# Performance work log

Measured on AMD Instinct MI355X. Metric: run time of the kernel, lower is better.

Reference implementation:

```python
import jax, jax.numpy as jnp
import numpy as np

EMBED_DIM = 1024
ATTN_DIM = 1024


def setup_inputs() -> dict:
    key = jax.random.key(0)
    k1, k2, k3, k4 = jax.random.split(key, 4)
    embedded = jax.random.normal(k1, (4, 2048, EMBED_DIM), dtype=jnp.float32)
    # torch nn.Linear weights are [out_features, in_features]
    s = 1.0 / np.sqrt(EMBED_DIM)
    Wk = jax.random.uniform(k2, (ATTN_DIM, EMBED_DIM), jnp.float32, -s, s)
    Wq = jax.random.uniform(k3, (ATTN_DIM, EMBED_DIM), jnp.float32, -s, s)
    Wv = jax.random.uniform(k4, (ATTN_DIM, EMBED_DIM), jnp.float32, -s, s)
    return {"embedded": embedded, "Wk": Wk, "Wq": Wq, "Wv": Wv}


def reference(embedded, Wk, Wq, Wv):
    # projections: x @ W.T  (torch Linear, no bias)
    k = jnp.einsum("bse,ae->bsa", embedded, Wk)
    q = jnp.einsum("bse,ae->bsa", embedded, Wq)
    v = jnp.einsum("bse,ae->bsa", embedded, Wv)
    scale = 1.0 / jnp.sqrt(jnp.float32(ATTN_DIM))
    attn = jnp.einsum("bqa,bka->bqk", q, k) * scale  # [B, S, S]
    S = attn.shape[1]
    causal = jnp.tril(jnp.ones((S, S), dtype=bool))
    attn = jnp.where(causal[None, :, :], attn, -jnp.inf)
    a = jax.nn.softmax(attn, axis=2)
    out = jnp.einsum("bqk,bka->bqa", a, v)
    return jnp.round(out, 4)
```

## Files before the change

kernel.cpp:

```cpp
#include <hip/hip_runtime.h>
#include <hip/hip_bf16.h>
#include <hip/hip_fp16.h>
#include <stdint.h>

typedef __bf16 bf16_t;
typedef bf16_t bf16x8 __attribute__((ext_vector_type(8)));
typedef bf16_t bf16x4 __attribute__((ext_vector_type(4)));
typedef _Float16 f16x8 __attribute__((ext_vector_type(8)));
typedef float f32x4 __attribute__((ext_vector_type(4)));

#define BM 128
#define BN 128
#define BK 32

__device__ __forceinline__ void gload_lds16(const void* g, void* l) {
    __builtin_amdgcn_global_load_lds(
        (const __attribute__((address_space(1))) void*)(uintptr_t)g,
        (__attribute__((address_space(3))) void*)(uintptr_t)l,
        16, 0, 0);
}

template <int EPI>
__device__ __forceinline__ void gemm_body(
    const bf16_t* __restrict__ A, long lda,
    const bf16_t* __restrict__ B, long ldb,
    void* __restrict__ Cv, long ldc,
    int k0beg, int k1end, float scale, int m0, int n0)
{
    __shared__ __align__(16) bf16_t As[BM * BK];
    __shared__ __align__(16) bf16_t Bs[BN * BK];

    const int tid = threadIdx.x;
    const int wid = tid >> 6, lane = tid & 63;
    const int wr = wid >> 1, wc = wid & 1;
    const int hw = lane >> 4, ln = lane & 15;

    const int ar0 = tid >> 2,         ak0 = (tid & 3) * 8;
    const int ar1 = (tid + 256) >> 2, ak1 = (tid & 3) * 8;

    const bf16_t* Arow0 = A + (size_t)(m0 + ar0) * lda + ak0;
    const bf16_t* Arow1 = A + (size_t)(m0 + ar1) * lda + ak1;
    const bf16_t* Brow0 = B + (size_t)(n0 + ar0) * ldb + ak0;
    const bf16_t* Brow1 = B + (size_t)(n0 + ar1) * ldb + ak1;

    f32x4 acc[4][4] = {};

    for (int k0 = k0beg; k0 < k1end; k0 += BK) {
        gload_lds16(Arow0 + k0, &As[wid * 512]);
        gload_lds16(Arow1 + k0, &As[2048 + wid * 512]);
        gload_lds16(Brow0 + k0, &Bs[wid * 512]);
        gload_lds16(Brow1 + k0, &Bs[2048 + wid * 512]);
        __syncthreads();

        bf16x8 af[4], bfr[4];
#pragma unroll
        for (int t = 0; t < 4; t++) {
            af[t]  = *(const bf16x8*)&As[(wr * 64 + t * 16 + ln) * BK + hw * 8];
            bfr[t] = *(const bf16x8*)&Bs[(wc * 64 + t * 16 + ln) * BK + hw * 8];
        }
#pragma unroll
        for (int ti = 0; ti < 4; ti++)
#pragma unroll
            for (int tj = 0; tj < 4; tj++)
                acc[ti][tj] = __builtin_amdgcn_mfma_f32_16x16x32_bf16(
                    af[ti], bfr[tj], acc[ti][tj], 0, 0, 0);
        __syncthreads();
    }

#pragma unroll
    for (int ti = 0; ti < 4; ti++) {
        const int rbase = m0 + wr * 64 + ti * 16 + hw * 4;
#pragma unroll
        for (int tj = 0; tj < 4; tj++) {
            const int col = n0 + wc * 64 + tj * 16 + ln;
#pragma unroll
            for (int rg = 0; rg < 4; rg++) {
                const float v = acc[ti][tj][rg] * scale;
                const size_t idx = (size_t)(rbase + rg) * ldc + col;
                if (EPI == 0)      ((bf16_t*)Cv)[idx]   = (bf16_t)v;
                else if (EPI == 1) ((_Float16*)Cv)[idx] = (_Float16)v;
                else               ((float*)Cv)[idx]    = v;
            }
        }
    }
}

__global__ __launch_bounds__(256) void gemm1_qkv(
    const bf16_t* __restrict__ xb, const bf16_t* __restrict__ Wb,
    bf16_t* __restrict__ QKVb)
{
    const int lin = blockIdx.x;
    const int xcd = lin & 7;
    const int j   = lin >> 3;
    const int p   = j >> 6;
    const int w   = j & 63;
    const int mblk = xcd * 8 + (w >> 3);
    const int nblk = p * 8 + (w & 7);
    gemm_body<0>(xb, 1024, Wb, 1024, QKVb, 3072,
                 0, 1024, 1.0f, mblk * BM, nblk * BN);
}

__global__ __launch_bounds__(256) void qk_vtrans(
    const bf16_t* __restrict__ QKVb, _Float16* __restrict__ S,
    bf16_t* __restrict__ Vt)
{
    const int id = blockIdx.x;
    if (id < 1024) {
        const int b  = id & 3;
        const int g  = id >> 2;
        const int my = 15 - (g >> 4);
        const int nx = g & 15;
        const int m0 = my * BM, n0 = nx * BN;
        if (n0 > m0 + (BM - 1)) return;
        const bf16_t* Qb = QKVb + 1024 + (size_t)b * (2048L * 3072);
        const bf16_t* Kb = QKVb + (size_t)b * (2048L * 3072);
        _Float16* Sb = S + (size_t)b * (2048L * 2048);
        gemm_body<1>(Qb, 3072, Kb, 3072, Sb, 2048, 0, 1024, 0.03125f, m0, n0);
    } else {
        __shared__ bf16_t ttile[32][33];
        const int t = id - 1024;
        const int b = t >> 11;
        const int lin = t & 2047;
        const int s0 = (lin & 63) * 32;
        const int d0 = (lin >> 6) * 32;
        const int tx = threadIdx.x & 31, ty = threadIdx.x >> 5;
#pragma unroll
        for (int k = 0; k < 4; k++) {
            const int s = s0 + ty + k * 8;
            const int d = d0 + tx;
            ttile[ty + k * 8][tx] = QKVb[(size_t)(b * 2048 + s) * 3072 + 2048 + d];
        }
        __syncthreads();
#pragma unroll
        for (int k = 0; k < 4; k++) {
            const int d = d0 + ty + k * 8;
            const int s = s0 + tx;
            Vt[(size_t)b * (1024 * 2048) + (size_t)d * 2048 + s] = ttile[tx][ty + k * 8];
        }
    }
}

__global__ __launch_bounds__(256) void gemm3_pv(
    const bf16_t* __restrict__ P, const bf16_t* __restrict__ Vt,
    float* __restrict__ out)
{
    const int id = blockIdx.x;
    const int strip = 15 - (id >> 5);
    const int nx = (id >> 2) & 7;
    const int b = id & 3;
    const int m0 = strip * BM;
    const int Keff = m0 + BM;
    gemm_body<2>(P + (size_t)b * (2048L * 2048), 2048,
                 Vt + (size_t)b * (1024L * 2048), 2048,
                 out + (size_t)b * (2048L * 1024), 1024,
                 0, Keff, 1.0f, m0, nx * BN);
}

__global__ __launch_bounds__(256) void cast_all(
    const float* __restrict__ x,
    const float* __restrict__ Wk, const float* __restrict__ Wq,
    const float* __restrict__ Wv,
    bf16_t* __restrict__ xb, bf16_t* __restrict__ Wb)
{
    const int blk = blockIdx.x;
    const float* src;
    bf16_t* dst;
    if (blk < 8192) {
        const size_t i = ((size_t)blk * 256 + threadIdx.x) * 4;
        src = x + i;
        dst = xb + i;
    } else {
        const size_t j = ((size_t)(blk - 8192) * 256 + threadIdx.x) * 4;
        dst = Wb + j;
        if (j < (size_t)1048576)      src = Wk + j;
        else if (j < (size_t)2097152) src = Wq + (j - 1048576);
        else                          src = Wv + (j - 2097152);
    }
    const float4 v = *(const float4*)src;
    bf16x4 o;
    o.x = (bf16_t)v.x; o.y = (bf16_t)v.y; o.z = (bf16_t)v.z; o.w = (bf16_t)v.w;
    *(bf16x4*)dst = o;
}

__device__ __forceinline__ float wred_max(float v) {
#pragma unroll
    for (int o = 32; o; o >>= 1) v = fmaxf(v, __shfl_xor(v, o, 64));
    return v;
}
__device__ __forceinline__ float wred_sum(float v) {
#pragma unroll
    for (int o = 32; o; o >>= 1) v += __shfl_xor(v, o, 64);
    return v;
}

__global__ __launch_bounds__(256) void softmax_rows(_Float16* __restrict__ S)
{
    __shared__ float red[8];
    const int r = blockIdx.x;
    const int i = r & 2047;
    const int n = i + 1;
    _Float16* row = S + (size_t)r * 2048;
    const int tid = threadIdx.x;
    const int wid = tid >> 6, lane = tid & 63;
    const int base = tid * 8;

    const f16x8 v8 = *(const f16x8*)(row + base);
    float vals[8];
    float mx = -3e30f;
#pragma unroll
    for (int k = 0; k < 8; k++) {
        const float v = (base + k < n) ? (float)v8[k] : -3e30f;
        vals[k] = v;
        mx = fmaxf(mx, v);
    }
    mx = wred_max(mx);
    if (lane == 0) red[wid] = mx;
    __syncthreads();
    mx = fmaxf(fmaxf(red[0], red[1]), fmaxf(red[2], red[3]));

    float s = 0.f;
#pragma unroll
    for (int k = 0; k < 8; k++) {
        const float e = __expf(vals[k] - mx);
        vals[k] = e;
        s += e;
    }
    s = wred_sum(s);
    if (lane == 0) red[4 + wid] = s;
    __syncthreads();
    s = red[4] + red[5] + red[6] + red[7];
    const float inv = 1.0f / s;

    bf16x8 o;
#pragma unroll
    for (int k = 0; k < 8; k++) o[k] = (bf16_t)(vals[k] * inv);
    *(bf16x8*)((bf16_t*)row + base) = o;
}

extern "C" void kernel_launch(void* const* d_in, const int* in_sizes, int n_in,
                              void* d_out, int out_size, void* d_ws, size_t ws_size,
                              hipStream_t stream)
{
    const float* x  = (const float*)d_in[0];
    const float* Wk = (const float*)d_in[1];
    const float* Wq = (const float*)d_in[2];
    const float* Wv = (const float*)d_in[3];
    char* ws = (char*)d_ws;

    bf16_t*   QKVb = (bf16_t*)(ws);
    bf16_t*   Vt   = (bf16_t*)(ws + ((size_t)48 << 20));
    bf16_t*   xb   = (bf16_t*)(ws + ((size_t)64 << 20));
    bf16_t*   Wb   = (bf16_t*)(ws + ((size_t)80 << 20));
    _Float16* S    = (_Float16*)(ws + ((size_t)64 << 20));
    float*    out  = (float*)d_out;

    cast_all<<<11264, 256, 0, stream>>>(x, Wk, Wq, Wv, xb, Wb);

    gemm1_qkv<<<1536, 256, 0, stream>>>(xb, Wb, QKVb);

    qk_vtrans<<<9216, 256, 0, stream>>>(QKVb, S, Vt);

    softmax_rows<<<8192, 256, 0, stream>>>(S);

    gemm3_pv<<<512, 256, 0, stream>>>((bf16_t*)S, Vt, out);
}
```

Measured before the change: 243.5 us.

## Widen GEMM tiles to 128x256, swizzle LDS, fuse V transpose into QKV epilogue

Widens the shared GEMM tile from 128x128 to 128x256, so each wave now computes 4x8 MFMA tiles, and adds an XOR-style rotation to the LDS layout to reduce bank conflicts. The V projection is written transposed straight from the QKV GEMM epilogue, which removes the separate transpose pass and the write and reread of V. The QK kernel now launches only causally needed tiles instead of launching all tiles and exiting early. The trade-offs are more accumulator registers, hence launch_bounds(256,2), and fewer blocks per launch, which may leave parts of the GPU idle.

```diff
diff --git a/kernel.cpp b/kernel.cpp
--- a/kernel.cpp
+++ b/kernel.cpp
@@ -10,7 +10,7 @@
 typedef float f32x4 __attribute__((ext_vector_type(4)));
 
 #define BM 128
-#define BN 128
+#define BN 256
 #define BK 32
 
 __device__ __forceinline__ void gload_lds16(const void* g, void* l) {
@@ -35,33 +35,48 @@
     const int wr = wid >> 1, wc = wid & 1;
     const int hw = lane >> 4, ln = lane & 15;
 
-    const int ar0 = tid >> 2,         ak0 = (tid & 3) * 8;
-    const int ar1 = (tid + 256) >> 2, ak1 = (tid & 3) * 8;
-
-    const bf16_t* Arow0 = A + (size_t)(m0 + ar0) * lda + ak0;
-    const bf16_t* Arow1 = A + (size_t)(m0 + ar1) * lda + ak1;
-    const bf16_t* Brow0 = B + (size_t)(n0 + ar0) * ldb + ak0;
-    const bf16_t* Brow1 = B + (size_t)(n0 + ar1) * ldb + ak1;
-
-    f32x4 acc[4][4] = {};
+    const bf16_t* srcA[2];
+#pragma unroll
+    for (int i = 0; i < 2; i++) {
+        const int c = tid + i * 256;
+        const int row = c >> 2;
+        const int j = ((c & 3) - (row >> 1)) & 3;
+        srcA[i] = A + (size_t)(m0 + row) * lda + j * 8;
+    }
+    const bf16_t* srcB[4];
+#pragma unroll
+    for (int q = 0; q < 4; q++) {
+        const int c = tid + q * 256;
+        const int row = c >> 2;
+        const int j = ((c & 3) - (row >> 1)) & 3;
+        srcB[q] = B + (size_t)(n0 + row) * ldb + j * 8;
+    }
+
+    f32x4 acc[4][8] = {};
 
     for (int k0 = k0beg; k0 < k1end; k0 += BK) {
-        gload_lds16(Arow0 + k0, &As[wid * 512]);
-        gload_lds16(Arow1 + k0, &As[2048 + wid * 512]);
-        gload_lds16(Brow0 + k0, &Bs[wid * 512]);
-        gload_lds16(Brow1 + k0, &Bs[2048 + wid * 512]);
+        gload_lds16(srcA[0] + k0, &As[wid * 512]);
+        gload_lds16(srcA[1] + k0, &As[2048 + wid * 512]);
+#pragma unroll
+        for (int q = 0; q < 4; q++)
+            gload_lds16(srcB[q] + k0, &Bs[q * 2048 + wid * 512]);
         __syncthreads();
 
-        bf16x8 af[4], bfr[4];
+        bf16x8 af[4], bfr[8];
 #pragma unroll
         for (int t = 0; t < 4; t++) {
-            af[t]  = *(const bf16x8*)&As[(wr * 64 + t * 16 + ln) * BK + hw * 8];
-            bfr[t] = *(const bf16x8*)&Bs[(wc * 64 + t * 16 + ln) * BK + hw * 8];
+            const int r = wr * 64 + t * 16 + ln;
+            af[t] = *(const bf16x8*)&As[r * BK + (((hw + (r >> 1)) & 3) * 8)];
         }
 #pragma unroll
+        for (int u = 0; u < 8; u++) {
+            const int rb = wc * 128 + u * 16 + ln;
+            bfr[u] = *(const bf16x8*)&Bs[rb * BK + (((hw + (rb >> 1)) & 3) * 8)];
+        }
+#pragma unroll
         for (int ti = 0; ti < 4; ti++)
 #pragma unroll
-            for (int tj = 0; tj < 4; tj++)
+            for (int tj = 0; tj < 8; tj++)
                 acc[ti][tj] = __builtin_amdgcn_mfma_f32_16x16x32_bf16(
                     af[ti], bfr[tj], acc[ti][tj], 0, 0, 0);
         __syncthreads();
@@ -71,89 +86,80 @@
     for (int ti = 0; ti < 4; ti++) {
         const int rbase = m0 + wr * 64 + ti * 16 + hw * 4;
 #pragma unroll
-        for (int tj = 0; tj < 4; tj++) {
-            const int col = n0 + wc * 64 + tj * 16 + ln;
-#pragma unroll
-            for (int rg = 0; rg < 4; rg++) {
-                const float v = acc[ti][tj][rg] * scale;
-                const size_t idx = (size_t)(rbase + rg) * ldc + col;
-                if (EPI == 0)      ((bf16_t*)Cv)[idx]   = (bf16_t)v;
-                else if (EPI == 1) ((_Float16*)Cv)[idx] = (_Float16)v;
-                else               ((float*)Cv)[idx]    = v;
+        for (int tj = 0; tj < 8; tj++) {
+            const int col = n0 + wc * 128 + tj * 16 + ln;
+            if (EPI == 4) {
+                const int bb = rbase >> 11;
+                const int s  = rbase & 2047;
+                const int d  = col - 2048;
+                bf16x4 o;
+#pragma unroll
+                for (int rg = 0; rg < 4; rg++) o[rg] = (bf16_t)acc[ti][tj][rg];
+                *(bf16x4*)&((bf16_t*)Cv)[(size_t)bb * 2097152 + (size_t)d * 2048 + s] = o;
+            } else {
+#pragma unroll
+                for (int rg = 0; rg < 4; rg++) {
+                    const float v = acc[ti][tj][rg] * scale;
+                    const size_t idx = (size_t)(rbase + rg) * ldc + col;
+                    if (EPI == 0)      ((bf16_t*)Cv)[idx]   = (bf16_t)v;
+                    else if (EPI == 1) ((_Float16*)Cv)[idx] = (_Float16)v;
+                    else               ((float*)Cv)[idx]    = v;
+                }
             }
         }
     }
 }
 
-__global__ __launch_bounds__(256) void gemm1_qkv(
+__global__ __launch_bounds__(256, 2) void gemm1_qkv(
     const bf16_t* __restrict__ xb, const bf16_t* __restrict__ Wb,
-    bf16_t* __restrict__ QKVb)
+    bf16_t* __restrict__ QKVb, bf16_t* __restrict__ Vt)
 {
     const int lin = blockIdx.x;
     const int xcd = lin & 7;
     const int j   = lin >> 3;
-    const int p   = j >> 6;
-    const int w   = j & 63;
-    const int mblk = xcd * 8 + (w >> 3);
-    const int nblk = p * 8 + (w & 7);
-    gemm_body<0>(xb, 1024, Wb, 1024, QKVb, 3072,
-                 0, 1024, 1.0f, mblk * BM, nblk * BN);
-}
-
-__global__ __launch_bounds__(256) void qk_vtrans(
-    const bf16_t* __restrict__ QKVb, _Float16* __restrict__ S,
-    bf16_t* __restrict__ Vt)
-{
-    const int id = blockIdx.x;
-    if (id < 1024) {
-        const int b  = id & 3;
-        const int g  = id >> 2;
-        const int my = 15 - (g >> 4);
-        const int nx = g & 15;
-        const int m0 = my * BM, n0 = nx * BN;
-        if (n0 > m0 + (BM - 1)) return;
-        const bf16_t* Qb = QKVb + 1024 + (size_t)b * (2048L * 3072);
-        const bf16_t* Kb = QKVb + (size_t)b * (2048L * 3072);
-        _Float16* Sb = S + (size_t)b * (2048L * 2048);
-        gemm_body<1>(Qb, 3072, Kb, 3072, Sb, 2048, 0, 1024, 0.03125f, m0, n0);
-    } else {
-        __shared__ bf16_t ttile[32][33];
-        const int t = id - 1024;
-        const int b = t >> 11;
-        const int lin = t & 2047;
-        const int s0 = (lin & 63) * 32;
-        const int d0 = (lin >> 6) * 32;
-        const int tx = threadIdx.x & 31, ty = threadIdx.x >> 5;
-#pragma unroll
-        for (int k = 0; k < 4; k++) {
-            const int s = s0 + ty + k * 8;
-            const int d = d0 + tx;
-            ttile[ty + k * 8][tx] = QKVb[(size_t)(b * 2048 + s) * 3072 + 2048 + d];
-        }
-        __syncthreads();
-#pragma unroll
-        for (int k = 0; k < 4; k++) {
-            const int d = d0 + ty + k * 8;
-            const int s = s0 + tx;
-            Vt[(size_t)b * (1024 * 2048) + (size_t)d * 2048 + s] = ttile[tx][ty + k * 8];
-        }
-    }
-}
-
-__global__ __launch_bounds__(256) void gemm3_pv(
+    const int p   = j >> 5;
+    const int w   = j & 31;
+    const int mblk = xcd * 8 + (w >> 2);
+    const int nblk = p * 4 + (w & 3);
+    const int m0 = mblk * BM, n0 = nblk * BN;
+    if (nblk < 8)
+        gemm_body<0>(xb, 1024, Wb, 1024, QKVb, 2048, 0, 1024, 1.0f, m0, n0);
+    else
+        gemm_body<4>(xb, 1024, Wb, 1024, Vt, 2048, 0, 1024, 1.0f, m0, n0);
+}
+
+__global__ __launch_bounds__(256, 2) void qk_gemm(
+    const bf16_t* __restrict__ QKVb, _Float16* __restrict__ S)
+{
+    const int b = blockIdx.x & 3;
+    int rem = blockIdx.x >> 2;
+    int my = 15, nx2 = 0;
+#pragma unroll
+    for (int m = 15; m >= 0; --m) {
+        const int c = (m >> 1) + 1;
+        if (rem < c) { my = m; nx2 = rem; break; }
+        rem -= c;
+    }
+    const bf16_t* base = QKVb + (size_t)b * (2048L * 2048);
+    gemm_body<1>(base + 1024, 2048,
+                 base, 2048,
+                 S + (size_t)b * (2048L * 2048), 2048,
+                 0, 1024, 0.03125f, my * BM, nx2 * BN);
+}
+
+__global__ __launch_bounds__(256, 2) void gemm3_pv(
     const bf16_t* __restrict__ P, const bf16_t* __restrict__ Vt,
     float* __restrict__ out)
 {
-    const int id = blockIdx.x;
-    const int strip = 15 - (id >> 5);
-    const int nx = (id >> 2) & 7;
-    const int b = id & 3;
+    const int b = blockIdx.x & 3;
+    const int g = blockIdx.x >> 2;
+    const int strip = 15 - (g >> 2);
+    const int nx2 = g & 3;
     const int m0 = strip * BM;
-    const int Keff = m0 + BM;
     gemm_body<2>(P + (size_t)b * (2048L * 2048), 2048,
                  Vt + (size_t)b * (1024L * 2048), 2048,
                  out + (size_t)b * (2048L * 1024), 1024,
-                 0, Keff, 1.0f, m0, nx * BN);
+                 0, m0 + BM, 1.0f, m0, nx2 * BN);
 }
 
 __global__ __launch_bounds__(256) void cast_all(
@@ -248,19 +254,19 @@
     char* ws = (char*)d_ws;
 
     bf16_t*   QKVb = (bf16_t*)(ws);
-    bf16_t*   Vt   = (bf16_t*)(ws + ((size_t)48 << 20));
-    bf16_t*   xb   = (bf16_t*)(ws + ((size_t)64 << 20));
-    bf16_t*   Wb   = (bf16_t*)(ws + ((size_t)80 << 20));
-    _Float16* S    = (_Float16*)(ws + ((size_t)64 << 20));
+    bf16_t*   Vt   = (bf16_t*)(ws + ((size_t)32 << 20));
+    bf16_t*   xb   = (bf16_t*)(ws + ((size_t)48 << 20));
+    bf16_t*   Wb   = (bf16_t*)(ws + ((size_t)64 << 20));
+    _Float16* S    = (_Float16*)(ws + ((size_t)48 << 20));
     float*    out  = (float*)d_out;
 
     cast_all<<<11264, 256, 0, stream>>>(x, Wk, Wq, Wv, xb, Wb);
 
-    gemm1_qkv<<<1536, 256, 0, stream>>>(xb, Wb, QKVb);
-
-    qk_vtrans<<<9216, 256, 0, stream>>>(QKVb, S, Vt);
+    gemm1_qkv<<<768, 256, 0, stream>>>(xb, Wb, QKVb, Vt);
+
+    qk_gemm<<<288, 256, 0, stream>>>(QKVb, S);
 
     softmax_rows<<<8192, 256, 0, stream>>>(S);
 
-    gemm3_pv<<<512, 256, 0, stream>>>((bf16_t*)S, Vt, out);
-}
+    gemm3_pv<<<256, 256, 0, stream>>>((bf16_t*)S, Vt, out);
+}
```

Result: slower. 266.7 us (+9.5%).
